# Kernel optimization log

Measured on AMD Instinct MI355X. Metric: run time of the kernel, lower is better.

The kernel has to match this reference:

```python
import jax, jax.numpy as jnp
import numpy as np

B, N, C_IN, F, OUT = 32, 1000, 128, 128, 64
RATIOS = (0.8, 0.8)


def setup_inputs() -> dict:
    key = jax.random.key(0)
    ks = jax.random.split(key, 10)
    N_nodes = jax.random.randint(ks[0], (B,), 500, N + 1, dtype=jnp.int32)
    ar = jnp.arange(N)
    mask = (ar[None, :] < N_nodes[:, None]).astype(jnp.float32)  # [B,N]
    A = (jax.random.uniform(ks[1], (B, N, N)) < 0.02).astype(jnp.float32)
    A = A * (1.0 - jnp.eye(N, dtype=jnp.float32))
    A = jnp.maximum(A, A.transpose(0, 2, 1))  # symmetric, no self loops
    A = A * mask[:, :, None] * mask[:, None, :]
    x = jax.random.normal(ks[2], (B, N, C_IN)) * mask[..., None]

    def lin(k, fin, fout):
        bnd = 1.0 / np.sqrt(fin)
        kw, kb = jax.random.split(k)
        W = jax.random.uniform(kw, (fout, fin), minval=-bnd, maxval=bnd)
        b = jax.random.uniform(kb, (fout,), minval=-bnd, maxval=bnd)
        return W, b

    W0, b0 = lin(ks[3], C_IN, F)
    W1, b1 = lin(ks[4], F, F)
    W2, b2 = lin(ks[5], F, F)
    bnd = 1.0 / np.sqrt(F)
    p0 = jax.random.uniform(ks[6], (F, 1), minval=-bnd, maxval=bnd)
    p1 = jax.random.uniform(ks[7], (F, 1), minval=-bnd, maxval=bnd)
    Wfc, bfc = lin(ks[8], F, OUT)
    return dict(x=x, A=A, mask=mask, N_nodes=N_nodes,
                W0=W0, b0=b0, W1=W1, b1=b1, W2=W2, b2=b2,
                p0=p0, p1=p1, Wfc=Wfc, bfc=bfc)


def _gconv(x, A, mask, W, b):
    # K=1 Kipf-Welling conv: L = D^-1/2 (A+I) D^-1/2; relu(Linear(L x)) * mask
    n = A.shape[1]
    A_hat = A + jnp.eye(n, dtype=A.dtype)
    D = (jnp.sum(A_hat, axis=1) + 1e-5) ** -0.5  # [B,N]
    L = D[:, :, None] * A_hat * D[:, None, :]
    h = jnp.einsum('bij,bjc->bic', L, x)
    h = h @ W.T + b
    return jax.nn.relu(h) * mask[..., None]


def _pool(x, A, mask, N_nodes, p, ratio):
    # score each node, drop the N_remove lowest-scoring valid nodes per graph
    y = (x @ p)[..., 0] / jnp.sqrt(jnp.sum(p ** 2))  # [B,N]
    N_remove = (N_nodes.astype(jnp.float32) * (1.0 - ratio)).astype(jnp.int32)
    y_key = jnp.where(mask > 0, y, jnp.inf)  # invalid nodes rank last
    ranks = jnp.argsort(jnp.argsort(y_key, axis=1), axis=1)  # ascending rank
    new_mask = ((ranks >= N_remove[:, None]) & (mask > 0)).astype(x.dtype)
    x = x * jnp.tanh(y)[..., None] * new_mask[..., None]
    A = new_mask[:, :, None] * A * new_mask[:, None, :]
    return x, A, new_mask, N_nodes - N_remove


def reference(x, A, mask, N_nodes, W0, b0, W1, b1, W2, b2, p0, p1, Wfc, bfc):
    h = _gconv(x, A, mask, W0, b0)
    h, A1, m1, n1 = _pool(h, A, mask, N_nodes, p0, RATIOS[0])
    h = _gconv(h, A1, m1, W1, b1)
    h, A2, m2, n2 = _pool(h, A1, m1, n1, p1, RATIOS[1])
    h = _gconv(h, A2, m2, W2, b2)
    g = jnp.max(h, axis=1)  # [B,F] global max pool
    return g @ Wfc.T + bfc  # [B,OUT]
```

## Files before the change

### kernel.cpp

```cpp
#include <hip/hip_runtime.h>
#include <math.h>

#define BB 32
#define NN 1000
#define CC 128
#define FF 128
#define OO 64
#define CAP 128
#define NB 40

#define RMC ((float)(1.0 - 0.8))

__global__ void k_csr(const float* __restrict__ A, const float* __restrict__ mask,
                      const int* __restrict__ Nn,
                      const float* __restrict__ p0, const float* __restrict__ p1,
                      const float* __restrict__ W0, const float* __restrict__ W1,
                      const float* __restrict__ W2,
                      short* __restrict__ idx, int* __restrict__ cnt,
                      float* __restrict__ D, float* __restrict__ dg,
                      float* __restrict__ m, float* __restrict__ gate,
                      int* __restrict__ ncur0, float* __restrict__ pn,
                      float* __restrict__ Wt){
  int i = blockIdx.x, b = blockIdx.y, lane = threadIdx.x;
  if (i == NN){
    for (int j = lane; j < NN; j += 64){
      float v = mask[b*NN + j]; m[b*NN + j] = v; gate[b*NN + j] = v;
    }
    if (lane == 0) ncur0[b] = Nn[b];
    if (b == 0 && lane == 1){ float s=0.f; for(int c=0;c<FF;c++) s += p0[c]*p0[c]; pn[0] = sqrtf(s); }
    if (b == 1 && lane == 1){ float s=0.f; for(int c=0;c<FF;c++) s += p1[c]*p1[c]; pn[1] = sqrtf(s); }
    for (int e = b*1536 + lane; e < (b+1)*1536; e += 64){
      int s = e / (FF*CC), rem = e % (FF*CC);
      int c = rem >> 7, f = rem & 127;
      const float* W = (s == 0) ? W0 : (s == 1) ? W1 : W2;
      Wt[(size_t)s*FF*CC + rem] = W[f*CC + c];
    }
    return;
  }
  if (mask[b*NN + i] == 0.f){
    if (lane == 0){
      cnt[b*NN + i] = 0;
      D[b*NN + i]  = 1.0f / sqrtf(1.0f + 1e-5f);
      dg[b*NN + i] = 0.f;
    }
    return;
  }
  const float4* row = (const float4*)(A + ((size_t)b*NN + i)*NN);
  short* out = idx + ((size_t)b*NN + i)*CAP;
  int count = 0;
  for (int base = 0; base < 250; base += 64){
    int q = base + lane;
    float4 v;
    if (q < 250) v = row[q]; else { v.x=v.y=v.z=v.w=0.f; }
    int lc = (v.x!=0.f) + (v.y!=0.f) + (v.z!=0.f) + (v.w!=0.f);
    int pre = lc;
    #pragma unroll
    for (int off = 1; off < 64; off <<= 1){
      int t = __shfl_up(pre, off);
      if (lane >= off) pre += t;
    }
    int tot = __shfl(pre, 63);
    pre -= lc;
    int slot = count + pre;
    int j = q*4;
    if (v.x!=0.f && slot < CAP) out[slot++] = (short)j;
    if (v.y!=0.f && slot < CAP) out[slot++] = (short)(j+1);
    if (v.z!=0.f && slot < CAP) out[slot++] = (short)(j+2);
    if (v.w!=0.f && slot < CAP) out[slot++] = (short)(j+3);
    count += tot;
  }
  if (lane == 0){
    int cn = (count < CAP) ? count : CAP;
    cnt[b*NN + i] = cn;
    float Dv = 1.0f / sqrtf((float)cn + 1.0f + 1e-5f);
    D[b*NN + i]  = Dv;
    dg[b*NN + i] = Dv;
  }
}

__global__ void k_aggt(const short* __restrict__ idx, const int* __restrict__ cnt,
                       const float* __restrict__ D, const float* __restrict__ dg,
                       const float* __restrict__ m, const float* __restrict__ gate,
                       const float* __restrict__ h, float* __restrict__ T){
  __shared__ int   nb[CAP];
  __shared__ float dn[CAP];
  __shared__ float red[4][CC];
  __shared__ int   wtot[2];
  int blk = blockIdx.x;
  int b = (blk & 7) + 8*((blk >> 3) & 3);
  int i = blk >> 5;
  int tid = threadIdx.x;
  size_t orow = ((size_t)b*NN + i)*CC;
  if (m[b*NN + i] == 0.f){
    T[orow + tid] = 0.f;
    return;
  }
  int n = cnt[b*NN + i];
  const short* r = idx + ((size_t)b*NN + i)*CAP;
  int j = 0; float d = 0.f; bool keep = false;
  if (tid < n){ j = (int)r[tid]; d = dg[b*NN + j]; keep = (d != 0.f); }
  unsigned long long ball = __ballot(keep);
  int lane64 = tid & 63, wv = tid >> 6;
  int pre = __popcll(ball & ((1ull << lane64) - 1ull));
  if (lane64 == 0) wtot[wv] = __popcll(ball);
  __syncthreads();
  int base = (wv == 1) ? wtot[0] : 0;
  if (keep){ nb[base + pre] = j*CC; dn[base + pre] = d; }
  int nlive = wtot[0] + wtot[1];
  int np = (nlive + 15) & ~15;
  for (int q = nlive + tid; q < np; q += 128){ nb[q] = 0; dn[q] = 0.f; }
  __syncthreads();
  int g = tid >> 5, lane = tid & 31;
  const float* hb = h + (size_t)b*NN*CC;
  float4 a0 = {0.f,0.f,0.f,0.f}, a1 = a0, a2 = a0, a3 = a0;
  for (int k = 0; k < np; k += 16){
    int e = k + g;
    float4 v0 = *(const float4*)(hb + nb[e   ] + (lane<<2));
    float4 v1 = *(const float4*)(hb + nb[e+ 4] + (lane<<2));
    float4 v2 = *(const float4*)(hb + nb[e+ 8] + (lane<<2));
    float4 v3 = *(const float4*)(hb + nb[e+12] + (lane<<2));
    float d0 = dn[e], d1 = dn[e+4], d2 = dn[e+8], d3 = dn[e+12];
    a0.x += d0*v0.x; a0.y += d0*v0.y; a0.z += d0*v0.z; a0.w += d0*v0.w;
    a1.x += d1*v1.x; a1.y += d1*v1.y; a1.z += d1*v1.z; a1.w += d1*v1.w;
    a2.x += d2*v2.x; a2.y += d2*v2.y; a2.z += d2*v2.z; a2.w += d2*v2.w;
    a3.x += d3*v3.x; a3.y += d3*v3.y; a3.z += d3*v3.z; a3.w += d3*v3.w;
  }
  float4 Yv;
  Yv.x = (a0.x + a1.x) + (a2.x + a3.x);
  Yv.y = (a0.y + a1.y) + (a2.y + a3.y);
  Yv.z = (a0.z + a1.z) + (a2.z + a3.z);
  Yv.w = (a0.w + a1.w) + (a2.w + a3.w);
  *(float4*)&red[g][lane<<2] = Yv;
  __syncthreads();
  int c = tid;
  float Y = (red[0][c] + red[1][c]) + (red[2][c] + red[3][c]);
  float Di = D[b*NN + i];
  float gi = gate[b*NN + i];
  T[orow + c] = Di*Y + Di*Di*(gi*hb[(size_t)i*CC + c]);
}

__global__ void k_lin(const float* __restrict__ T, const float* __restrict__ m,
                      const float* __restrict__ Wt,
                      const float* __restrict__ bias, float* __restrict__ Hout){
  __shared__ float t[NB][CC];
  int b = blockIdx.y, tid = threadIdx.x;
  int i0 = blockIdx.x * NB;
  const float4* Tg = (const float4*)(T + ((size_t)b*NN + i0)*CC);
  float4* tl = (float4*)&t[0][0];
  #pragma unroll
  for (int e = 0; e < 5; e++) tl[tid + e*256] = Tg[tid + e*256];
  __syncthreads();
  int fg = tid & 31;
  int nr = tid >> 5;
  float acc[5][4];
  float4 bi = ((const float4*)bias)[fg];
  #pragma unroll
  for (int n5 = 0; n5 < 5; n5++){
    acc[n5][0]=bi.x; acc[n5][1]=bi.y; acc[n5][2]=bi.z; acc[n5][3]=bi.w;
  }
  for (int c4 = 0; c4 < 32; c4++){
    float4 tv[5];
    #pragma unroll
    for (int n5 = 0; n5 < 5; n5++)
      tv[n5] = *((const float4*)&t[nr + n5*8][c4*4]);
    #pragma unroll
    for (int k = 0; k < 4; k++){
      float4 wv = ((const float4*)Wt)[(size_t)(c4*4 + k)*32 + fg];
      #pragma unroll
      for (int n5 = 0; n5 < 5; n5++){
        float tvv = (k==0) ? tv[n5].x : (k==1) ? tv[n5].y : (k==2) ? tv[n5].z : tv[n5].w;
        acc[n5][0] += tvv*wv.x; acc[n5][1] += tvv*wv.y;
        acc[n5][2] += tvv*wv.z; acc[n5][3] += tvv*wv.w;
      }
    }
  }
  #pragma unroll
  for (int n5 = 0; n5 < 5; n5++){
    int i = i0 + nr + n5*8;
    float mi = m[b*NN + i];
    float4 o4;
    o4.x = fmaxf(acc[n5][0], 0.f)*mi;
    o4.y = fmaxf(acc[n5][1], 0.f)*mi;
    o4.z = fmaxf(acc[n5][2], 0.f)*mi;
    o4.w = fmaxf(acc[n5][3], 0.f)*mi;
    ((float4*)&Hout[((size_t)b*NN + i)*CC])[fg] = o4;
  }
}

__global__ void k_score(const float* __restrict__ H, const float* __restrict__ p,
                        const float* __restrict__ pn, float* __restrict__ y){
  int i = blockIdx.x, b = blockIdx.y, lane = threadIdx.x;
  const float* hrow = H + ((size_t)b*NN + i)*CC;
  float s = hrow[lane]*p[lane] + hrow[lane+64]*p[lane+64];
  for (int off = 32; off > 0; off >>= 1) s += __shfl_down(s, off);
  if (lane == 0) y[b*NN + i] = s / pn[0];
}

__global__ void k_pool(const float* __restrict__ y, float* __restrict__ m,
                       const int* __restrict__ ncur_in, int* __restrict__ ncur_out,
                       float* __restrict__ gate){
  __shared__ float yk[NN];
  int b = blockIdx.y, tid = threadIdx.x;
  int i = blockIdx.x*256 + tid;
  for (int j = tid; j < NN; j += 256)
    yk[j] = (m[b*NN + j] > 0.f) ? y[b*NN + j] : INFINITY;
  __syncthreads();
  int n = ncur_in[b];
  int nr = (int)((float)n * RMC);
  float myv = (i < NN) ? yk[i] : INFINITY;
  int cnt = 0;
  const float4* yk4 = (const float4*)yk;
  #pragma unroll 5
  for (int q = 0; q < 250; q++){
    float4 v = yk4[q];
    int j0 = q*4;
    cnt += (int)((v.x < myv) || (v.x == myv && j0     < i));
    cnt += (int)((v.y < myv) || (v.y == myv && j0 + 1 < i));
    cnt += (int)((v.z < myv) || (v.z == myv && j0 + 2 < i));
    cnt += (int)((v.w < myv) || (v.w == myv && j0 + 3 < i));
  }
  if (i < NN){
    bool keep = (cnt >= nr) && (m[b*NN + i] > 0.f);
    m[b*NN + i]    = keep ? 1.0f : 0.0f;
    gate[b*NN + i] = keep ? tanhf(y[b*NN + i]) : 0.0f;
  }
  if (blockIdx.x == 0 && tid == 0) ncur_out[b] = n - nr;
}

__global__ void k_deg(const short* __restrict__ idx, const int* __restrict__ cnt,
                      const float* __restrict__ m, const float* __restrict__ gate,
                      float* __restrict__ D, float* __restrict__ dg){
  __shared__ float ml[NN];
  int b = blockIdx.y, tid = threadIdx.x;
  for (int i = tid; i < NN; i += 256) ml[i] = m[b*NN + i];
  __syncthreads();
  int j = blockIdx.x*250 + tid;
  if (tid < 250){
    const short* r = idx + ((size_t)b*NN + j)*CAP;
    int n = cnt[b*NN + j];
    float s0=0.f, s1=0.f, s2=0.f, s3=0.f;
    int k = 0;
    for (; k+4 <= n; k += 4){
      s0 += ml[r[k]]; s1 += ml[r[k+1]]; s2 += ml[r[k+2]]; s3 += ml[r[k+3]];
    }
    for (; k < n; k++) s0 += ml[r[k]];
    float Dv = 1.0f / sqrtf(((s0+s1)+(s2+s3)) + 1.0f + 1e-5f);
    D[b*NN + j]  = Dv;
    dg[b*NN + j] = Dv * gate[b*NN + j];
  }
}

__global__ void k_fmax(const float* __restrict__ H, const float* __restrict__ m,
                       float* __restrict__ part){
  int sx = blockIdx.x, b = blockIdx.y, c = threadIdx.x;
  float mx = 0.f;
  int i0 = sx*125;
  for (int i = i0; i < i0+125; i++){
    if (m[b*NN + i] != 0.f)
      mx = fmaxf(mx, H[((size_t)b*NN + i)*CC + c]);
  }
  part[((size_t)b*8 + sx)*CC + c] = mx;
}

__global__ void k_fc(const float* __restrict__ part, const float* __restrict__ Wfc,
                     const float* __restrict__ bfc, float* __restrict__ out){
  __shared__ float g[FF];
  int b = blockIdx.x, tid = threadIdx.x;
  float mx = 0.f;
  #pragma unroll
  for (int s = 0; s < 8; s++) mx = fmaxf(mx, part[((size_t)b*8 + s)*CC + tid]);
  g[tid] = mx;
  __syncthreads();
  if (tid < OO){
    float acc = bfc[tid];
    for (int c = 0; c < FF; c++) acc += g[c]*Wfc[tid*FF + c];
    out[b*OO + tid] = acc;
  }
}

extern "C" void kernel_launch(void* const* d_in, const int* in_sizes, int n_in,
                              void* d_out, int out_size, void* d_ws, size_t ws_size,
                              hipStream_t stream) {
  const float* x    = (const float*)d_in[0];
  const float* A    = (const float*)d_in[1];
  const float* mask = (const float*)d_in[2];
  const int*   Nn   = (const int*)  d_in[3];
  const float* W0   = (const float*)d_in[4];
  const float* b0   = (const float*)d_in[5];
  const float* W1   = (const float*)d_in[6];
  const float* b1   = (const float*)d_in[7];
  const float* W2   = (const float*)d_in[8];
  const float* b2   = (const float*)d_in[9];
  const float* p0   = (const float*)d_in[10];
  const float* p1   = (const float*)d_in[11];
  const float* Wfc  = (const float*)d_in[12];
  const float* bfc  = (const float*)d_in[13];
  float* out = (float*)d_out;

  char* w = (char*)d_ws;
  float* H   = (float*)w; w += (size_t)BB*NN*CC*4;
  float* T   = (float*)w; w += (size_t)BB*NN*CC*4;
  short* idx = (short*)w; w += (size_t)BB*NN*CAP*2;
  float* Wt  = (float*)w; w += (size_t)3*FF*CC*4;
  float* part= (float*)w; w += (size_t)8*BB*CC*4;
  int*   cnt = (int*)w;   w += (size_t)BB*NN*4;
  float* D   = (float*)w; w += (size_t)BB*NN*4;
  float* m   = (float*)w; w += (size_t)BB*NN*4;
  float* ysc = (float*)w; w += (size_t)BB*NN*4;
  float* gate= (float*)w; w += (size_t)BB*NN*4;
  float* dg  = (float*)w; w += (size_t)BB*NN*4;
  int*   ncur= (int*)w;   w += 3*BB*sizeof(int);
  float* pn  = (float*)w; w += 64;

  k_csr<<<dim3(NN + 1, BB), 64, 0, stream>>>(A, mask, Nn, p0, p1, W0, W1, W2,
                                             idx, cnt, D, dg, m, gate, ncur, pn, Wt);

  k_aggt<<<BB*NN, 128, 0, stream>>>(idx, cnt, D, dg, m, gate, x, T);
  k_lin<<<dim3(25, BB), 256, 0, stream>>>(T, m, Wt + 0*FF*CC, b0, H);
  k_score<<<dim3(NN, BB), 64, 0, stream>>>(H, p0, pn + 0, ysc);
  k_pool<<<dim3(4, BB), 256, 0, stream>>>(ysc, m, ncur + 0*BB, ncur + 1*BB, gate);
  k_deg<<<dim3(4, BB), 256, 0, stream>>>(idx, cnt, m, gate, D, dg);

  k_aggt<<<BB*NN, 128, 0, stream>>>(idx, cnt, D, dg, m, gate, H, T);
  k_lin<<<dim3(25, BB), 256, 0, stream>>>(T, m, Wt + 1*FF*CC, b1, H);
  k_score<<<dim3(NN, BB), 64, 0, stream>>>(H, p1, pn + 1, ysc);
  k_pool<<<dim3(4, BB), 256, 0, stream>>>(ysc, m, ncur + 1*BB, ncur + 2*BB, gate);
  k_deg<<<dim3(4, BB), 256, 0, stream>>>(idx, cnt, m, gate, D, dg);

  k_aggt<<<BB*NN, 128, 0, stream>>>(idx, cnt, D, dg, m, gate, H, T);
  k_lin<<<dim3(25, BB), 256, 0, stream>>>(T, m, Wt + 2*FF*CC, b2, H);

  k_fmax<<<dim3(8, BB), 128, 0, stream>>>(H, m, part);
  k_fc<<<BB, 128, 0, stream>>>(part, Wfc, bfc, out);
}
```

Measured before the change: 465.7 us.

## Map one wavefront per node in sparse aggregation, removing block barriers

The aggregation kernel now handles four nodes per 256-thread block, one 64-lane wavefront per node, instead of one node per 128-thread block. Neighbor compaction uses per-wave ballots and wave barriers, and the final reduction uses a cross-half shuffle instead of shared-memory reduction with __syncthreads. The aim is to cut synchronization and launch overhead and to pad neighbor lists to 8 rather than 16. In exchange each node gets fewer lanes for its gather, and only half the wave writes the output.

```diff
diff --git a/kernel.cpp b/kernel.cpp
--- a/kernel.cpp
+++ b/kernel.cpp
@@ -82,61 +82,75 @@
                        const float* __restrict__ D, const float* __restrict__ dg,
                        const float* __restrict__ m, const float* __restrict__ gate,
                        const float* __restrict__ h, float* __restrict__ T){
-  __shared__ int   nb[CAP];
-  __shared__ float dn[CAP];
-  __shared__ float red[4][CC];
-  __shared__ int   wtot[2];
+  __shared__ int   nb[4][CAP];
+  __shared__ float dn[4][CAP];
   int blk = blockIdx.x;
-  int b = (blk & 7) + 8*((blk >> 3) & 3);
-  int i = blk >> 5;
+  int b   = (blk & 7) + 8*((blk >> 3) & 3);
+  int rem = blk >> 5;
   int tid = threadIdx.x;
+  int w = tid >> 6, lane = tid & 63;
+  int i = rem*4 + w;
+  int g = lane >> 5, l32 = lane & 31;
   size_t orow = ((size_t)b*NN + i)*CC;
+  const float* hb = h + (size_t)b*NN*CC;
   if (m[b*NN + i] == 0.f){
-    T[orow + tid] = 0.f;
+    if (g == 0){ float4 z = {0.f,0.f,0.f,0.f}; *(float4*)(T + orow + (l32<<2)) = z; }
     return;
   }
   int n = cnt[b*NN + i];
   const short* r = idx + ((size_t)b*NN + i)*CAP;
-  int j = 0; float d = 0.f; bool keep = false;
-  if (tid < n){ j = (int)r[tid]; d = dg[b*NN + j]; keep = (d != 0.f); }
-  unsigned long long ball = __ballot(keep);
-  int lane64 = tid & 63, wv = tid >> 6;
-  int pre = __popcll(ball & ((1ull << lane64) - 1ull));
-  if (lane64 == 0) wtot[wv] = __popcll(ball);
-  __syncthreads();
-  int base = (wv == 1) ? wtot[0] : 0;
-  if (keep){ nb[base + pre] = j*CC; dn[base + pre] = d; }
-  int nlive = wtot[0] + wtot[1];
-  int np = (nlive + 15) & ~15;
-  for (int q = nlive + tid; q < np; q += 128){ nb[q] = 0; dn[q] = 0.f; }
-  __syncthreads();
-  int g = tid >> 5, lane = tid & 31;
-  const float* hb = h + (size_t)b*NN*CC;
+  int*   nbw = nb[w];
+  float* dnw = dn[w];
+  int j0 = 0; float d0 = 0.f; bool k0 = false;
+  if (lane < n){ j0 = (int)r[lane]; d0 = dg[b*NN + j0]; k0 = (d0 != 0.f); }
+  unsigned long long bal = __ballot(k0);
+  int pre = __popcll(bal & ((1ull << lane) - 1ull));
+  if (k0){ nbw[pre] = j0*CC; dnw[pre] = d0; }
+  int nlive = __popcll(bal);
+  if (n > 64){
+    int e = lane + 64; int j1 = 0; float d1 = 0.f; bool k1 = false;
+    if (e < n){ j1 = (int)r[e]; d1 = dg[b*NN + j1]; k1 = (d1 != 0.f); }
+    unsigned long long bal1 = __ballot(k1);
+    int pre1 = __popcll(bal1 & ((1ull << lane) - 1ull));
+    if (k1){ nbw[nlive + pre1] = j1*CC; dnw[nlive + pre1] = d1; }
+    nlive += __popcll(bal1);
+  }
+  int np = (nlive + 7) & ~7;
+  if (lane < np - nlive){ nbw[nlive + lane] = 0; dnw[nlive + lane] = 0.f; }
+  __builtin_amdgcn_wave_barrier();
   float4 a0 = {0.f,0.f,0.f,0.f}, a1 = a0, a2 = a0, a3 = a0;
-  for (int k = 0; k < np; k += 16){
+  for (int k = 0; k < np; k += 8){
     int e = k + g;
-    float4 v0 = *(const float4*)(hb + nb[e   ] + (lane<<2));
-    float4 v1 = *(const float4*)(hb + nb[e+ 4] + (lane<<2));
-    float4 v2 = *(const float4*)(hb + nb[e+ 8] + (lane<<2));
-    float4 v3 = *(const float4*)(hb + nb[e+12] + (lane<<2));
-    float d0 = dn[e], d1 = dn[e+4], d2 = dn[e+8], d3 = dn[e+12];
-    a0.x += d0*v0.x; a0.y += d0*v0.y; a0.z += d0*v0.z; a0.w += d0*v0.w;
-    a1.x += d1*v1.x; a1.y += d1*v1.y; a1.z += d1*v1.z; a1.w += d1*v1.w;
-    a2.x += d2*v2.x; a2.y += d2*v2.y; a2.z += d2*v2.z; a2.w += d2*v2.w;
-    a3.x += d3*v3.x; a3.y += d3*v3.y; a3.z += d3*v3.z; a3.w += d3*v3.w;
-  }
-  float4 Yv;
-  Yv.x = (a0.x + a1.x) + (a2.x + a3.x);
-  Yv.y = (a0.y + a1.y) + (a2.y + a3.y);
-  Yv.z = (a0.z + a1.z) + (a2.z + a3.z);
-  Yv.w = (a0.w + a1.w) + (a2.w + a3.w);
-  *(float4*)&red[g][lane<<2] = Yv;
-  __syncthreads();
-  int c = tid;
-  float Y = (red[0][c] + red[1][c]) + (red[2][c] + red[3][c]);
+    float4 v0 = *(const float4*)(hb + nbw[e  ] + (l32<<2));
+    float4 v1 = *(const float4*)(hb + nbw[e+2] + (l32<<2));
+    float4 v2 = *(const float4*)(hb + nbw[e+4] + (l32<<2));
+    float4 v3 = *(const float4*)(hb + nbw[e+6] + (l32<<2));
+    float e0 = dnw[e], e1 = dnw[e+2], e2 = dnw[e+4], e3 = dnw[e+6];
+    a0.x += e0*v0.x; a0.y += e0*v0.y; a0.z += e0*v0.z; a0.w += e0*v0.w;
+    a1.x += e1*v1.x; a1.y += e1*v1.y; a1.z += e1*v1.z; a1.w += e1*v1.w;
+    a2.x += e2*v2.x; a2.y += e2*v2.y; a2.z += e2*v2.z; a2.w += e2*v2.w;
+    a3.x += e3*v3.x; a3.y += e3*v3.y; a3.z += e3*v3.z; a3.w += e3*v3.w;
+  }
+  float4 Y;
+  Y.x = (a0.x + a1.x) + (a2.x + a3.x);
+  Y.y = (a0.y + a1.y) + (a2.y + a3.y);
+  Y.z = (a0.z + a1.z) + (a2.z + a3.z);
+  Y.w = (a0.w + a1.w) + (a2.w + a3.w);
+  Y.x += __shfl_xor(Y.x, 32);
+  Y.y += __shfl_xor(Y.y, 32);
+  Y.z += __shfl_xor(Y.z, 32);
+  Y.w += __shfl_xor(Y.w, 32);
   float Di = D[b*NN + i];
   float gi = gate[b*NN + i];
-  T[orow + c] = Di*Y + Di*Di*(gi*hb[(size_t)i*CC + c]);
+  if (g == 0){
+    float4 hv = *(const float4*)(hb + (size_t)i*CC + (l32<<2));
+    float4 o;
+    o.x = Di*Y.x + Di*Di*(gi*hv.x);
+    o.y = Di*Y.y + Di*Di*(gi*hv.y);
+    o.z = Di*Y.z + Di*Di*(gi*hv.z);
+    o.w = Di*Y.w + Di*Di*(gi*hv.w);
+    *(float4*)(T + orow + (l32<<2)) = o;
+  }
 }
 
 __global__ void k_lin(const float* __restrict__ T, const float* __restrict__ m,
@@ -315,19 +329,19 @@
   k_csr<<<dim3(NN + 1, BB), 64, 0, stream>>>(A, mask, Nn, p0, p1, W0, W1, W2,
                                              idx, cnt, D, dg, m, gate, ncur, pn, Wt);
 
-  k_aggt<<<BB*NN, 128, 0, stream>>>(idx, cnt, D, dg, m, gate, x, T);
+  k_aggt<<<(BB*NN)/4, 256, 0, stream>>>(idx, cnt, D, dg, m, gate, x, T);
   k_lin<<<dim3(25, BB), 256, 0, stream>>>(T, m, Wt + 0*FF*CC, b0, H);
   k_score<<<dim3(NN, BB), 64, 0, stream>>>(H, p0, pn + 0, ysc);
   k_pool<<<dim3(4, BB), 256, 0, stream>>>(ysc, m, ncur + 0*BB, ncur + 1*BB, gate);
   k_deg<<<dim3(4, BB), 256, 0, stream>>>(idx, cnt, m, gate, D, dg);
 
-  k_aggt<<<BB*NN, 128, 0, stream>>>(idx, cnt, D, dg, m, gate, H, T);
+  k_aggt<<<(BB*NN)/4, 256, 0, stream>>>(idx, cnt, D, dg, m, gate, H, T);
   k_lin<<<dim3(25, BB), 256, 0, stream>>>(T, m, Wt + 1*FF*CC, b1, H);
   k_score<<<dim3(NN, BB), 64, 0, stream>>>(H, p1, pn + 1, ysc);
   k_pool<<<dim3(4, BB), 256, 0, stream>>>(ysc, m, ncur + 1*BB, ncur + 2*BB, gate);
   k_deg<<<dim3(4, BB), 256, 0, stream>>>(idx, cnt, m, gate, D, dg);
 
-  k_aggt<<<BB*NN, 128, 0, stream>>>(idx, cnt, D, dg, m, gate, H, T);
+  k_aggt<<<(BB*NN)/4, 256, 0, stream>>>(idx, cnt, D, dg, m, gate, H, T);
   k_lin<<<dim3(25, BB), 256, 0, stream>>>(T, m, Wt + 2*FF*CC, b2, H);
 
   k_fmax<<<dim3(8, BB), 128, 0, stream>>>(H, m, part);
```

Result: no change. 465.2 us (-0.1%).
